# Kernel optimization log

Hardware: AMD Instinct MI355X
Metric: run time of the kernel (lower is better)

The kernel has to match this reference:

```python
import jax, jax.numpy as jnp
import numpy as np

D_MODEL = 1024
N_HEADS = 16
D_K = D_MODEL // N_HEADS


def setup_inputs() -> dict:
    key = jax.random.key(0)
    ks = jax.random.split(key, 9)
    s = 0.02
    x = jax.random.normal(ks[0], (2, 2048, D_MODEL), dtype=jnp.float32)
    Wq = jax.random.normal(ks[1], (D_MODEL, D_MODEL), dtype=jnp.float32) * s
    bq = jax.random.normal(ks[2], (D_MODEL,), dtype=jnp.float32) * s
    Wk = jax.random.normal(ks[3], (D_MODEL, D_MODEL), dtype=jnp.float32) * s
    bk = jax.random.normal(ks[4], (D_MODEL,), dtype=jnp.float32) * s
    Wv = jax.random.normal(ks[5], (D_MODEL, D_MODEL), dtype=jnp.float32) * s
    bv = jax.random.normal(ks[6], (D_MODEL,), dtype=jnp.float32) * s
    Wo = jax.random.normal(ks[7], (D_MODEL, D_MODEL), dtype=jnp.float32) * s
    bo = jax.random.normal(ks[8], (D_MODEL,), dtype=jnp.float32) * s
    return {"x": x, "Wq": Wq, "bq": bq, "Wk": Wk, "bk": bk,
            "Wv": Wv, "bv": bv, "Wo": Wo, "bo": bo}


def reference(x, Wq, bq, Wk, bk, Wv, bv, Wo, bo):
    B, S, D = x.shape
    # nn.Linear: y = x @ W.T + b
    q = x @ Wq.T + bq  # [B,S,D]
    k = x @ Wk.T + bk
    v = x @ Wv.T + bv
    # split heads -> [B,H,S,dk]
    q = q.reshape(B, S, N_HEADS, D_K).transpose(0, 2, 1, 3)
    k = k.reshape(B, S, N_HEADS, D_K).transpose(0, 2, 1, 3)
    v = v.reshape(B, S, N_HEADS, D_K).transpose(0, 2, 1, 3)
    scale = 1.0 / jnp.sqrt(jnp.asarray(D_K, dtype=x.dtype))
    scores = jnp.einsum('bhqd,bhkd->bhqk', q, k) * scale  # [B,H,S,S]
    weights = jax.nn.softmax(scores, axis=-1)
    out = jnp.einsum('bhqk,bhkd->bhqd', weights, v)  # [B,H,S,dk]
    concat = out.transpose(0, 2, 1, 3).reshape(B, S, D)
    return concat @ Wo.T + bo
```

## Files before the change

### kernel.cpp

```cpp
#include <hip/hip_runtime.h>

typedef unsigned short ushort_t;
typedef __attribute__((ext_vector_type(8))) __bf16 bf16x8;
typedef __attribute__((ext_vector_type(4))) float floatx4;

#define AS1 __attribute__((address_space(1)))
#define AS3 __attribute__((address_space(3)))

#define D_MODEL 1024
#define NH 16
#define DKH 64
#define SEQ 2048
#define NB 2
#define MTOT (NB * SEQ)

#define QSCALE 0.18033688011112042f

#define OFF_X   0u
#define OFF_WQ  4194304u
#define OFF_BQ  5242880u
#define OFF_WK  5243904u
#define OFF_BK  6292480u
#define OFF_WV  6293504u
#define OFF_BV  7342080u
#define OFF_WO  7343104u
#define OFF_BO  8391680u
#define CVT_TOT 8392704u

__device__ __forceinline__ float bf2f(ushort_t u) {
    union { unsigned u; float f; } v; v.u = ((unsigned)u) << 16; return v.f;
}
__device__ __forceinline__ ushort_t f2bf(float f) {
    union { float f; unsigned u; } v; v.f = f;
    unsigned r = v.u + 0x7FFFu + ((v.u >> 16) & 1u);
    return (ushort_t)(r >> 16);
}
__device__ __forceinline__ unsigned pack2bf(float a, float b) {
    unsigned ua = __float_as_uint(a), ub = __float_as_uint(b);
    ua = ua + 0x7FFFu + ((ua >> 16) & 1u);
    ub = ub + 0x7FFFu + ((ub >> 16) & 1u);
    return __builtin_amdgcn_perm(ub, ua, 0x07060302);
}
__device__ __forceinline__ float fexp2(float x) { return __builtin_amdgcn_exp2f(x); }

#define GSYNC(N) do { \
    asm volatile("s_waitcnt vmcnt(" #N ")" ::: "memory"); \
    __builtin_amdgcn_s_barrier(); \
    __builtin_amdgcn_sched_barrier(0); \
} while (0)

__global__ __launch_bounds__(256) void convert_kernel(
    const float* __restrict__ x,  const float* __restrict__ wq, const float* __restrict__ bq_,
    const float* __restrict__ wk, const float* __restrict__ bk_, const float* __restrict__ wv,
    const float* __restrict__ bv_, const float* __restrict__ wo, const float* __restrict__ bo_,
    ushort_t* __restrict__ dst)
{
    const unsigned idx = ((unsigned)blockIdx.x * 256u + threadIdx.x) * 4u;
    if (idx >= CVT_TOT) return;
    const float* src; unsigned off;
    if      (idx < OFF_WQ) { src = x;   off = idx - OFF_X;  }
    else if (idx < OFF_BQ) { src = wq;  off = idx - OFF_WQ; }
    else if (idx < OFF_WK) { src = bq_; off = idx - OFF_BQ; }
    else if (idx < OFF_BK) { src = wk;  off = idx - OFF_WK; }
    else if (idx < OFF_WV) { src = bk_; off = idx - OFF_BK; }
    else if (idx < OFF_BV) { src = wv;  off = idx - OFF_WV; }
    else if (idx < OFF_WO) { src = bv_; off = idx - OFF_BV; }
    else if (idx < OFF_BO) { src = wo;  off = idx - OFF_WO; }
    else                   { src = bo_; off = idx - OFF_BO; }
    float4 v = *reinterpret_cast<const float4*>(src + off);
    uint2 p;
    p.x = pack2bf(v.x, v.y);
    p.y = pack2bf(v.z, v.w);
    *reinterpret_cast<uint2*>(dst + idx) = p;
}

__device__ __forceinline__ void gemm_core(
    const ushort_t* __restrict__ X, const ushort_t* __restrict__ W,
    int m0, int n0, ushort_t* lds, floatx4 acc[4][4])
{
    const int tid = threadIdx.x;
    const int lane = tid & 63, wv = tid >> 6;
    const int wm = (wv >> 1) * 64, wn = (wv & 1) * 64;
    const int l15 = lane & 15, quad = lane >> 4;
    const floatx4 z4 = {0.f, 0.f, 0.f, 0.f};
#pragma unroll
    for (int i = 0; i < 4; ++i)
#pragma unroll
        for (int j = 0; j < 4; ++j) acc[i][j] = z4;
    const int lrow = lane >> 2;
    const int lcol = (lane & 3) * 8;
    const ushort_t* gA = X + (size_t)(m0 + lrow) * D_MODEL + lcol;
    const ushort_t* gB = W + (size_t)(n0 + lrow) * D_MODEL + lcol;

    auto STAGE = [&](ushort_t* Ln, int k0) {
#pragma unroll
        for (int j = 0; j < 2; ++j) {
            const int r0 = (wv * 2 + j) * 16;
            __builtin_amdgcn_global_load_lds(
                (const AS1 unsigned*)(gA + (size_t)r0 * D_MODEL + k0),
                (AS3 unsigned*)(Ln + r0 * 32), 16, 0, 0);
            __builtin_amdgcn_global_load_lds(
                (const AS1 unsigned*)(gB + (size_t)r0 * D_MODEL + k0),
                (AS3 unsigned*)(Ln + 4096 + r0 * 32), 16, 0, 0);
        }
    };
    auto COMPUTE = [&](const ushort_t* L) {
        bf16x8 af[4], bfr[4];
#pragma unroll
        for (int i = 0; i < 4; ++i)
            af[i] = *reinterpret_cast<const bf16x8*>(L + (wm + i * 16 + l15) * 32 + quad * 8);
#pragma unroll
        for (int j = 0; j < 4; ++j)
            bfr[j] = *reinterpret_cast<const bf16x8*>(L + 4096 + (wn + j * 16 + l15) * 32 + quad * 8);
#pragma unroll
        for (int i = 0; i < 4; ++i)
#pragma unroll
            for (int j = 0; j < 4; ++j)
                acc[i][j] = __builtin_amdgcn_mfma_f32_16x16x32_bf16(af[i], bfr[j], acc[i][j], 0, 0, 0);
    };

    ushort_t* b0 = lds;
    ushort_t* b1 = lds + 8192;
    ushort_t* b2 = lds + 16384;

    STAGE(b0, 0);
    STAGE(b1, 32);
    for (int tt = 0; tt < 30; tt += 3) {
        GSYNC(4); STAGE(b2, (tt + 2) * 32); COMPUTE(b0);
        GSYNC(4); STAGE(b0, (tt + 3) * 32); COMPUTE(b1);
        GSYNC(4); STAGE(b1, (tt + 4) * 32); COMPUTE(b2);
    }
    GSYNC(4); COMPUTE(b0);
    GSYNC(0); COMPUTE(b1);
}

__global__ __launch_bounds__(256, 3) void qkv_kernel(
    const ushort_t* __restrict__ x,
    const ushort_t* __restrict__ Wq, const ushort_t* __restrict__ bq,
    const ushort_t* __restrict__ Wk, const ushort_t* __restrict__ bk,
    const ushort_t* __restrict__ Wv, const ushort_t* __restrict__ bv,
    ushort_t* __restrict__ q_ws, ushort_t* __restrict__ k_ws, ushort_t* __restrict__ vt_ws)
{
    __shared__ __align__(16) ushort_t lds[24576];
    const int L = blockIdx.x;
    const int m_idx = (L & 7) + 8 * ((L >> 3) & 3);
    const int y = L >> 5;
    const int m0 = m_idx * 128;
    const int which = y >> 3;
    const int n0 = (y & 7) * 128;
    const ushort_t* W    = (which == 0) ? Wq : (which == 1) ? Wk : Wv;
    const ushort_t* bias = (which == 0) ? bq : (which == 1) ? bk : bv;
    floatx4 acc[4][4];
    gemm_core(x, W, m0, n0, lds, acc);
    const int tid = threadIdx.x, lane = tid & 63, wv = tid >> 6;
    const int wm = (wv >> 1) * 64, wn = (wv & 1) * 64;
    const int l15 = lane & 15, quad = lane >> 4;
    const int b0 = m0 >> 11;
    const int s0 = m0 & (SEQ - 1);
    __syncthreads();
    if (which < 2) {
        ushort_t* Ts = lds;
        ushort_t* dst = (which == 0) ? q_ws : k_ws;
        const float scl = (which == 0) ? QSCALE : 1.0f;
#pragma unroll
        for (int j = 0; j < 4; ++j) {
            int coln = wn + j * 16 + l15;
            float bb = bf2f(bias[n0 + coln]);
#pragma unroll
            for (int i = 0; i < 4; ++i)
#pragma unroll
                for (int r = 0; r < 4; ++r) {
                    int rowm = wm + i * 16 + quad * 4 + r;
                    Ts[rowm * 136 + coln] = f2bf((acc[i][j][r] + bb) * scl);
                }
        }
        __syncthreads();
#pragma unroll
        for (int i = 0; i < 8; ++i) {
            int c = tid + 256 * i;
            int rowm = c >> 4, chunk = c & 15;
            float4 v = *reinterpret_cast<const float4*>(Ts + rowm * 136 + chunk * 8);
            int s = s0 + rowm;
            int n = n0 + chunk * 8, h = n >> 6, d = n & 63;
            *reinterpret_cast<float4*>(dst + (((size_t)(b0 * NH + h)) * SEQ + s) * DKH + d) = v;
        }
    } else {
        ushort_t* Ts = lds;
#pragma unroll
        for (int j = 0; j < 4; ++j) {
            int coln = wn + j * 16 + l15;
            float bb = bf2f(bias[n0 + coln]);
#pragma unroll
            for (int i = 0; i < 4; ++i)
#pragma unroll
                for (int r = 0; r < 4; ++r) {
                    int rowm = wm + i * 16 + quad * 4 + r;
                    Ts[coln * 136 + rowm] = f2bf(acc[i][j][r] + bb);
                }
        }
        __syncthreads();
#pragma unroll
        for (int i = 0; i < 8; ++i) {
            int c = tid + 256 * i;
            int nr = c >> 4, mc = (c & 15) * 8;
            float4 v = *reinterpret_cast<const float4*>(Ts + nr * 136 + mc);
            int n = n0 + nr, h = n >> 6, d = n & 63;
            *reinterpret_cast<float4*>(vt_ws + (((size_t)(b0 * NH + h)) * DKH + d) * SEQ + s0 + mc) = v;
        }
    }
}

__global__ __launch_bounds__(512, 4) void attn_kernel(
    const ushort_t* __restrict__ q_ws, const ushort_t* __restrict__ k_ws,
    const ushort_t* __restrict__ vt_ws, ushort_t* __restrict__ concat)
{
    __shared__ __align__(16) ushort_t sm[36864];
    const int L = blockIdx.x;
    const int qb = (L >> 3) & 15;
    const int bh = (L & 7) + ((L >> 7) << 3);
    const int tid = threadIdx.x;
    const int lane = tid & 63, wv = tid >> 6;
    const int half = wv >> 2, wq = wv & 3;
    const int l15 = lane & 15, quad = lane >> 4;
    const int ht = tid & 255;

    const ushort_t* Qg = q_ws + ((size_t)bh * SEQ + qb * 128) * DKH;
    const ushort_t* Kg = k_ws + ((size_t)bh * SEQ + half * (SEQ / 2)) * DKH;
    const ushort_t* Vg = vt_ws + (size_t)bh * DKH * SEQ + half * (SEQ / 2);

    ushort_t* Ks     = sm + half * 4608;
    ushort_t* VTs    = sm + 9216 + half * 4608;
    ushort_t* Ps     = sm + 18432 + wv * 2304;
    ushort_t* Qstage = sm + 18432;

    const int r0c = ht >> 3,         c0c = (ht & 7) * 8;
    const int r1c = (ht + 256) >> 3, c1c = ((ht + 256) & 7) * 8;

#pragma unroll
    for (int i = 0; i < 2; ++i) {
        int c = tid + 512 * i;
        int row = c >> 3, col = (c & 7) * 8;
        *reinterpret_cast<float4*>(Qstage + row * 72 + col) =
            *reinterpret_cast<const float4*>(Qg + row * DKH + col);
    }
    __syncthreads();
    bf16x8 aq[2][2];
#pragma unroll
    for (int nt = 0; nt < 2; ++nt)
#pragma unroll
        for (int ks = 0; ks < 2; ++ks)
            aq[nt][ks] = *reinterpret_cast<const bf16x8*>(Qstage + (wq * 32 + nt * 16 + l15) * 72 + ks * 32 + quad * 8);

    const floatx4 z4 = {0.f, 0.f, 0.f, 0.f};
    floatx4 o[2][4];
    floatx4 la4[2] = {z4, z4};
#pragma unroll
    for (int nt = 0; nt < 2; ++nt)
#pragma unroll
        for (int dt = 0; dt < 4; ++dt) o[nt][dt] = z4;

    float4 pk0 = *reinterpret_cast<const float4*>(Kg + (size_t)r0c * DKH + c0c);
    float4 pk1 = *reinterpret_cast<const float4*>(Kg + (size_t)r1c * DKH + c1c);
    float4 pv0 = *reinterpret_cast<const float4*>(Vg + (size_t)r0c * SEQ + c0c);
    float4 pv1 = *reinterpret_cast<const float4*>(Vg + (size_t)r1c * SEQ + c1c);

    for (int t = 0; t < 16; ++t) {
        __syncthreads();
        *reinterpret_cast<float4*>(Ks + r0c * 72 + c0c) = pk0;
        *reinterpret_cast<float4*>(Ks + r1c * 72 + c1c) = pk1;
        *reinterpret_cast<float4*>(VTs + r0c * 72 + c0c) = pv0;
        *reinterpret_cast<float4*>(VTs + r1c * 72 + c1c) = pv1;
        __syncthreads();
        if (t < 15) {
            int toff = (t + 1) * 64;
            pk0 = *reinterpret_cast<const float4*>(Kg + (size_t)(toff + r0c) * DKH + c0c);
            pk1 = *reinterpret_cast<const float4*>(Kg + (size_t)(toff + r1c) * DKH + c1c);
            pv0 = *reinterpret_cast<const float4*>(Vg + (size_t)r0c * SEQ + toff + c0c);
            pv1 = *reinterpret_cast<const float4*>(Vg + (size_t)r1c * SEQ + toff + c1c);
        }

        floatx4 st[2][4];
#pragma unroll
        for (int mt = 0; mt < 4; ++mt) {
            bf16x8 akf = *reinterpret_cast<const bf16x8*>(Ks + (mt * 16 + l15) * 72 + quad * 8);
            st[0][mt] = __builtin_amdgcn_mfma_f32_16x16x32_bf16(akf, aq[0][0], z4, 0, 0, 0);
            st[1][mt] = __builtin_amdgcn_mfma_f32_16x16x32_bf16(akf, aq[1][0], z4, 0, 0, 0);
        }
#pragma unroll
        for (int mt = 0; mt < 4; ++mt) {
            bf16x8 akf = *reinterpret_cast<const bf16x8*>(Ks + (mt * 16 + l15) * 72 + 32 + quad * 8);
            st[0][mt] = __builtin_amdgcn_mfma_f32_16x16x32_bf16(akf, aq[0][1], st[0][mt], 0, 0, 0);
            st[1][mt] = __builtin_amdgcn_mfma_f32_16x16x32_bf16(akf, aq[1][1], st[1][mt], 0, 0, 0);
        }

#pragma unroll
        for (int nt = 0; nt < 2; ++nt)
#pragma unroll
            for (int mt = 0; mt < 4; ++mt) {
#pragma unroll
                for (int r = 0; r < 4; ++r) st[nt][mt][r] = fexp2(st[nt][mt][r]);
                la4[nt] += st[nt][mt];
                uint2 pk;
                pk.x = pack2bf(st[nt][mt][0], st[nt][mt][1]);
                pk.y = pack2bf(st[nt][mt][2], st[nt][mt][3]);
                *reinterpret_cast<uint2*>(Ps + (nt * 16 + l15) * 72 + mt * 16 + quad * 4) = pk;
            }
        asm volatile("s_waitcnt lgkmcnt(0)" ::: "memory");
#pragma unroll
        for (int ks = 0; ks < 2; ++ks) {
            bf16x8 ap0 = *reinterpret_cast<const bf16x8*>(Ps + l15 * 72 + ks * 32 + quad * 8);
            bf16x8 ap1 = *reinterpret_cast<const bf16x8*>(Ps + (16 + l15) * 72 + ks * 32 + quad * 8);
#pragma unroll
            for (int dt = 0; dt < 4; ++dt) {
                bf16x8 bvv = *reinterpret_cast<const bf16x8*>(VTs + (dt * 16 + l15) * 72 + ks * 32 + quad * 8);
                o[0][dt] = __builtin_amdgcn_mfma_f32_16x16x32_bf16(ap0, bvv, o[0][dt], 0, 0, 0);
                o[1][dt] = __builtin_amdgcn_mfma_f32_16x16x32_bf16(ap1, bvv, o[1][dt], 0, 0, 0);
            }
        }
    }
    float lsum[2];
#pragma unroll
    for (int nt = 0; nt < 2; ++nt) {
        float s = la4[nt][0] + la4[nt][1] + la4[nt][2] + la4[nt][3];
        s += __shfl_xor(s, 16, 64);
        s += __shfl_xor(s, 32, 64);
        lsum[nt] = s;
    }
    __syncthreads();
    float* Of = (float*)sm;
    float* lf = Of + 128 * 68;
    if (half == 1) {
#pragma unroll
        for (int nt = 0; nt < 2; ++nt) {
            if (quad == 0) lf[wq * 32 + nt * 16 + l15] = lsum[nt];
#pragma unroll
            for (int r = 0; r < 4; ++r) {
                int row = wq * 32 + nt * 16 + quad * 4 + r;
#pragma unroll
                for (int dt = 0; dt < 4; ++dt)
                    Of[row * 68 + dt * 16 + l15] = o[nt][dt][r];
            }
        }
    }
    __syncthreads();
    if (half == 0) {
        const int b0 = bh >> 4, h = bh & 15;
#pragma unroll
        for (int nt = 0; nt < 2; ++nt) {
            float ltot = lsum[nt] + lf[wq * 32 + nt * 16 + l15];
            float linv = 1.f / ltot;
#pragma unroll
            for (int r = 0; r < 4; ++r) {
                float lB = __shfl(linv, quad * 4 + r, 64);
                int row = wq * 32 + nt * 16 + quad * 4 + r;
                size_t base = ((size_t)(b0 * SEQ + qb * 128 + row)) * D_MODEL + h * DKH;
#pragma unroll
                for (int dt = 0; dt < 4; ++dt) {
                    float sum = o[nt][dt][r] + Of[row * 68 + dt * 16 + l15];
                    concat[base + dt * 16 + l15] = f2bf(sum * lB);
                }
            }
        }
    }
}

__global__ __launch_bounds__(256, 3) void oproj_kernel(
    const ushort_t* __restrict__ cc, const ushort_t* __restrict__ Wo,
    const ushort_t* __restrict__ bo, float* __restrict__ out)
{
    __shared__ __align__(16) ushort_t lds[24576];
    const int L = blockIdx.x;
    const int m_idx = (L & 7) + 8 * (L >> 6);
    const int n_idx = (L >> 3) & 7;
    const int m0 = m_idx * 128, n0 = n_idx * 128;
    floatx4 acc[4][4];
    gemm_core(cc, Wo, m0, n0, lds, acc);
    const int tid = threadIdx.x, lane = tid & 63, wv = tid >> 6;
    const int wm = (wv >> 1) * 64, wn = (wv & 1) * 64;
    const int l15 = lane & 15, quad = lane >> 4;
#pragma unroll
    for (int j = 0; j < 4; ++j) {
        int n = n0 + wn + j * 16 + l15;
        float bb = bf2f(bo[n]);
#pragma unroll
        for (int i = 0; i < 4; ++i)
#pragma unroll
            for (int r = 0; r < 4; ++r) {
                int m = m0 + wm + i * 16 + quad * 4 + r;
                out[(size_t)m * D_MODEL + n] = acc[i][j][r] + bb;
            }
    }
}

extern "C" void kernel_launch(void* const* d_in, const int* in_sizes, int n_in,
                              void* d_out, int out_size, void* d_ws, size_t ws_size,
                              hipStream_t stream)
{
    ushort_t* cvt = (ushort_t*)d_ws;
    const ushort_t* xb  = cvt + OFF_X;
    const ushort_t* Wqb = cvt + OFF_WQ;
    const ushort_t* bqb = cvt + OFF_BQ;
    const ushort_t* Wkb = cvt + OFF_WK;
    const ushort_t* bkb = cvt + OFF_BK;
    const ushort_t* Wvb = cvt + OFF_WV;
    const ushort_t* bvb = cvt + OFF_BV;
    const ushort_t* Wob = cvt + OFF_WO;
    const ushort_t* bob = cvt + OFF_BO;
    ushort_t* q_ws   = cvt + CVT_TOT;
    ushort_t* k_ws   = q_ws  + (size_t)MTOT * D_MODEL;
    ushort_t* vt_ws  = k_ws  + (size_t)MTOT * D_MODEL;
    ushort_t* concat = vt_ws + (size_t)MTOT * D_MODEL;

    convert_kernel<<<(CVT_TOT / 1024), 256, 0, stream>>>(
        (const float*)d_in[0], (const float*)d_in[1], (const float*)d_in[2],
        (const float*)d_in[3], (const float*)d_in[4], (const float*)d_in[5],
        (const float*)d_in[6], (const float*)d_in[7], (const float*)d_in[8], cvt);
    qkv_kernel<<<dim3(768), 256, 0, stream>>>(xb, Wqb, bqb, Wkb, bkb, Wvb, bvb, q_ws, k_ws, vt_ws);
    attn_kernel<<<dim3(512), 512, 0, stream>>>(q_ws, k_ws, vt_ws, concat);
    oproj_kernel<<<dim3(256), 256, 0, stream>>>(concat, Wob, bob, (float*)d_out);
}
```

Baseline: 190.2 us.

## Enlarge QKV GEMM tiles to 256x128 and use eight-wave blocks for output projection

The QKV projection now runs 512-thread blocks that each compute a 256x128 tile, with triple-buffered LDS stages sized for the taller A tile. A new block-to-tile mapping assigns consecutive N tiles to the same XCD so x rows are shared within an XCD's cache. The output projection keeps 128x128 tiles but spreads them over eight waves, each computing 64x32, which gives more latency hiding per block. The larger QKV tiles reuse each B tile across more rows, but they halve the block count to 384, which may load the CUs unevenly, and they raise LDS use per block.

New measurement: 193.2 us. No clear change (+1.6%).

```diff
diff --git a/kernel.cpp b/kernel.cpp
--- a/kernel.cpp
+++ b/kernel.cpp
@@ -74,7 +74,7 @@
     *reinterpret_cast<uint2*>(dst + idx) = p;
 }
 
-__device__ __forceinline__ void gemm_core(
+__device__ __forceinline__ void gemm_core_qkv(
     const ushort_t* __restrict__ X, const ushort_t* __restrict__ W,
     int m0, int n0, ushort_t* lds, floatx4 acc[4][4])
 {
@@ -95,14 +95,15 @@
     auto STAGE = [&](ushort_t* Ln, int k0) {
 #pragma unroll
         for (int j = 0; j < 2; ++j) {
-            const int r0 = (wv * 2 + j) * 16;
+            const int rA = (wv * 2 + j) * 16;
             __builtin_amdgcn_global_load_lds(
-                (const AS1 unsigned*)(gA + (size_t)r0 * D_MODEL + k0),
-                (AS3 unsigned*)(Ln + r0 * 32), 16, 0, 0);
-            __builtin_amdgcn_global_load_lds(
-                (const AS1 unsigned*)(gB + (size_t)r0 * D_MODEL + k0),
-                (AS3 unsigned*)(Ln + 4096 + r0 * 32), 16, 0, 0);
-        }
+                (const AS1 unsigned*)(gA + (size_t)rA * D_MODEL + k0),
+                (AS3 unsigned*)(Ln + rA * 32), 16, 0, 0);
+        }
+        const int rB = wv * 16;
+        __builtin_amdgcn_global_load_lds(
+            (const AS1 unsigned*)(gB + (size_t)rB * D_MODEL + k0),
+            (AS3 unsigned*)(Ln + 8192 + rB * 32), 16, 0, 0);
     };
     auto COMPUTE = [&](const ushort_t* L) {
         bf16x8 af[4], bfr[4];
@@ -111,7 +112,7 @@
             af[i] = *reinterpret_cast<const bf16x8*>(L + (wm + i * 16 + l15) * 32 + quad * 8);
 #pragma unroll
         for (int j = 0; j < 4; ++j)
-            bfr[j] = *reinterpret_cast<const bf16x8*>(L + 4096 + (wn + j * 16 + l15) * 32 + quad * 8);
+            bfr[j] = *reinterpret_cast<const bf16x8*>(L + 8192 + (wn + j * 16 + l15) * 32 + quad * 8);
 #pragma unroll
         for (int i = 0; i < 4; ++i)
 #pragma unroll
@@ -120,38 +121,39 @@
     };
 
     ushort_t* b0 = lds;
-    ushort_t* b1 = lds + 8192;
-    ushort_t* b2 = lds + 16384;
-
+    ushort_t* b1 = lds + 12288;
+    ushort_t* b2 = lds + 24576;
     STAGE(b0, 0);
     STAGE(b1, 32);
     for (int tt = 0; tt < 30; tt += 3) {
-        GSYNC(4); STAGE(b2, (tt + 2) * 32); COMPUTE(b0);
-        GSYNC(4); STAGE(b0, (tt + 3) * 32); COMPUTE(b1);
-        GSYNC(4); STAGE(b1, (tt + 4) * 32); COMPUTE(b2);
-    }
-    GSYNC(4); COMPUTE(b0);
+        GSYNC(3); STAGE(b2, (tt + 2) * 32); COMPUTE(b0);
+        GSYNC(3); STAGE(b0, (tt + 3) * 32); COMPUTE(b1);
+        GSYNC(3); STAGE(b1, (tt + 4) * 32); COMPUTE(b2);
+    }
+    GSYNC(3); COMPUTE(b0);
     GSYNC(0); COMPUTE(b1);
 }
 
-__global__ __launch_bounds__(256, 3) void qkv_kernel(
+__global__ __launch_bounds__(512, 2) void qkv_kernel(
     const ushort_t* __restrict__ x,
     const ushort_t* __restrict__ Wq, const ushort_t* __restrict__ bq,
     const ushort_t* __restrict__ Wk, const ushort_t* __restrict__ bk,
     const ushort_t* __restrict__ Wv, const ushort_t* __restrict__ bv,
     ushort_t* __restrict__ q_ws, ushort_t* __restrict__ k_ws, ushort_t* __restrict__ vt_ws)
 {
-    __shared__ __align__(16) ushort_t lds[24576];
+    __shared__ __align__(16) ushort_t lds[36864];
     const int L = blockIdx.x;
-    const int m_idx = (L & 7) + 8 * ((L >> 3) & 3);
-    const int y = L >> 5;
-    const int m0 = m_idx * 128;
-    const int which = y >> 3;
-    const int n0 = (y & 7) * 128;
+    const int xcd = L & 7;
+    const int r = L >> 3;
+    const int n_idx = xcd * 3 + (r % 3);
+    const int m_idx = r / 3;
+    const int m0 = m_idx * 256;
+    const int which = n_idx >> 3;
+    const int n0 = (n_idx & 7) * 128;
     const ushort_t* W    = (which == 0) ? Wq : (which == 1) ? Wk : Wv;
     const ushort_t* bias = (which == 0) ? bq : (which == 1) ? bk : bv;
     floatx4 acc[4][4];
-    gemm_core(x, W, m0, n0, lds, acc);
+    gemm_core_qkv(x, W, m0, n0, lds, acc);
     const int tid = threadIdx.x, lane = tid & 63, wv = tid >> 6;
     const int wm = (wv >> 1) * 64, wn = (wv & 1) * 64;
     const int l15 = lane & 15, quad = lane >> 4;
@@ -169,15 +171,15 @@
 #pragma unroll
             for (int i = 0; i < 4; ++i)
 #pragma unroll
-                for (int r = 0; r < 4; ++r) {
-                    int rowm = wm + i * 16 + quad * 4 + r;
-                    Ts[rowm * 136 + coln] = f2bf((acc[i][j][r] + bb) * scl);
+                for (int rr = 0; rr < 4; ++rr) {
+                    int rowm = wm + i * 16 + quad * 4 + rr;
+                    Ts[rowm * 136 + coln] = f2bf((acc[i][j][rr] + bb) * scl);
                 }
         }
         __syncthreads();
 #pragma unroll
         for (int i = 0; i < 8; ++i) {
-            int c = tid + 256 * i;
+            int c = tid + 512 * i;
             int rowm = c >> 4, chunk = c & 15;
             float4 v = *reinterpret_cast<const float4*>(Ts + rowm * 136 + chunk * 8);
             int s = s0 + rowm;
@@ -193,17 +195,17 @@
 #pragma unroll
             for (int i = 0; i < 4; ++i)
 #pragma unroll
-                for (int r = 0; r < 4; ++r) {
-                    int rowm = wm + i * 16 + quad * 4 + r;
-                    Ts[coln * 136 + rowm] = f2bf(acc[i][j][r] + bb);
+                for (int rr = 0; rr < 4; ++rr) {
+                    int rowm = wm + i * 16 + quad * 4 + rr;
+                    Ts[coln * 264 + rowm] = f2bf(acc[i][j][rr] + bb);
                 }
         }
         __syncthreads();
 #pragma unroll
         for (int i = 0; i < 8; ++i) {
-            int c = tid + 256 * i;
-            int nr = c >> 4, mc = (c & 15) * 8;
-            float4 v = *reinterpret_cast<const float4*>(Ts + nr * 136 + mc);
+            int c = tid + 512 * i;
+            int nr = c >> 5, mc = (c & 31) * 8;
+            float4 v = *reinterpret_cast<const float4*>(Ts + nr * 264 + mc);
             int n = n0 + nr, h = n >> 6, d = n & 63;
             *reinterpret_cast<float4*>(vt_ws + (((size_t)(b0 * NH + h)) * DKH + d) * SEQ + s0 + mc) = v;
         }
@@ -298,7 +300,7 @@
 #pragma unroll
             for (int mt = 0; mt < 4; ++mt) {
 #pragma unroll
-                for (int r = 0; r < 4; ++r) st[nt][mt][r] = fexp2(st[nt][mt][r]);
+                for (int rr = 0; rr < 4; ++rr) st[nt][mt][rr] = fexp2(st[nt][mt][rr]);
                 la4[nt] += st[nt][mt];
                 uint2 pk;
                 pk.x = pack2bf(st[nt][mt][0], st[nt][mt][1]);
@@ -334,11 +336,11 @@
         for (int nt = 0; nt < 2; ++nt) {
             if (quad == 0) lf[wq * 32 + nt * 16 + l15] = lsum[nt];
 #pragma unroll
-            for (int r = 0; r < 4; ++r) {
-                int row = wq * 32 + nt * 16 + quad * 4 + r;
+            for (int rr = 0; rr < 4; ++rr) {
+                int row = wq * 32 + nt * 16 + quad * 4 + rr;
 #pragma unroll
                 for (int dt = 0; dt < 4; ++dt)
-                    Of[row * 68 + dt * 16 + l15] = o[nt][dt][r];
+                    Of[row * 68 + dt * 16 + l15] = o[nt][dt][rr];
             }
         }
     }
@@ -350,13 +352,13 @@
             float ltot = lsum[nt] + lf[wq * 32 + nt * 16 + l15];
             float linv = 1.f / ltot;
 #pragma unroll
-            for (int r = 0; r < 4; ++r) {
-                float lB = __shfl(linv, quad * 4 + r, 64);
-                int row = wq * 32 + nt * 16 + quad * 4 + r;
+            for (int rr = 0; rr < 4; ++rr) {
+                float lB = __shfl(linv, quad * 4 + rr, 64);
+                int row = wq * 32 + nt * 16 + quad * 4 + rr;
                 size_t base = ((size_t)(b0 * SEQ + qb * 128 + row)) * D_MODEL + h * DKH;
 #pragma unroll
                 for (int dt = 0; dt < 4; ++dt) {
-                    float sum = o[nt][dt][r] + Of[row * 68 + dt * 16 + l15];
+                    float sum = o[nt][dt][rr] + Of[row * 68 + dt * 16 + l15];
                     concat[base + dt * 16 + l15] = f2bf(sum * lB);
                 }
             }
@@ -364,30 +366,76 @@
     }
 }
 
-__global__ __launch_bounds__(256, 3) void oproj_kernel(
+__global__ __launch_bounds__(512, 2) void oproj_kernel(
     const ushort_t* __restrict__ cc, const ushort_t* __restrict__ Wo,
     const ushort_t* __restrict__ bo, float* __restrict__ out)
 {
     __shared__ __align__(16) ushort_t lds[24576];
     const int L = blockIdx.x;
-    const int m_idx = (L & 7) + 8 * (L >> 6);
-    const int n_idx = (L >> 3) & 7;
-    const int m0 = m_idx * 128, n0 = n_idx * 128;
-    floatx4 acc[4][4];
-    gemm_core(cc, Wo, m0, n0, lds, acc);
-    const int tid = threadIdx.x, lane = tid & 63, wv = tid >> 6;
-    const int wm = (wv >> 1) * 64, wn = (wv & 1) * 64;
+    const int n0 = (L & 7) * 128;
+    const int m0 = (L >> 3) * 128;
+    const int tid = threadIdx.x;
+    const int lane = tid & 63, wv = tid >> 6;
+    const int wm = (wv >> 2) * 64, wn = (wv & 3) * 32;
     const int l15 = lane & 15, quad = lane >> 4;
-#pragma unroll
-    for (int j = 0; j < 4; ++j) {
+    const floatx4 z4 = {0.f, 0.f, 0.f, 0.f};
+    floatx4 acc[4][2];
+#pragma unroll
+    for (int i = 0; i < 4; ++i)
+#pragma unroll
+        for (int j = 0; j < 2; ++j) acc[i][j] = z4;
+    const int lrow = lane >> 2;
+    const int lcol = (lane & 3) * 8;
+    const ushort_t* gA = cc + (size_t)(m0 + lrow) * D_MODEL + lcol;
+    const ushort_t* gB = Wo + (size_t)(n0 + lrow) * D_MODEL + lcol;
+
+    auto STAGE = [&](ushort_t* Ln, int k0) {
+        const int r0 = wv * 16;
+        __builtin_amdgcn_global_load_lds(
+            (const AS1 unsigned*)(gA + (size_t)r0 * D_MODEL + k0),
+            (AS3 unsigned*)(Ln + r0 * 32), 16, 0, 0);
+        __builtin_amdgcn_global_load_lds(
+            (const AS1 unsigned*)(gB + (size_t)r0 * D_MODEL + k0),
+            (AS3 unsigned*)(Ln + 4096 + r0 * 32), 16, 0, 0);
+    };
+    auto COMPUTE = [&](const ushort_t* Lb) {
+        bf16x8 af[4], bfr[2];
+#pragma unroll
+        for (int i = 0; i < 4; ++i)
+            af[i] = *reinterpret_cast<const bf16x8*>(Lb + (wm + i * 16 + l15) * 32 + quad * 8);
+#pragma unroll
+        for (int j = 0; j < 2; ++j)
+            bfr[j] = *reinterpret_cast<const bf16x8*>(Lb + 4096 + (wn + j * 16 + l15) * 32 + quad * 8);
+#pragma unroll
+        for (int i = 0; i < 4; ++i)
+#pragma unroll
+            for (int j = 0; j < 2; ++j)
+                acc[i][j] = __builtin_amdgcn_mfma_f32_16x16x32_bf16(af[i], bfr[j], acc[i][j], 0, 0, 0);
+    };
+
+    ushort_t* b0 = lds;
+    ushort_t* b1 = lds + 8192;
+    ushort_t* b2 = lds + 16384;
+    STAGE(b0, 0);
+    STAGE(b1, 32);
+    for (int tt = 0; tt < 30; tt += 3) {
+        GSYNC(2); STAGE(b2, (tt + 2) * 32); COMPUTE(b0);
+        GSYNC(2); STAGE(b0, (tt + 3) * 32); COMPUTE(b1);
+        GSYNC(2); STAGE(b1, (tt + 4) * 32); COMPUTE(b2);
+    }
+    GSYNC(2); COMPUTE(b0);
+    GSYNC(0); COMPUTE(b1);
+
+#pragma unroll
+    for (int j = 0; j < 2; ++j) {
         int n = n0 + wn + j * 16 + l15;
         float bb = bf2f(bo[n]);
 #pragma unroll
         for (int i = 0; i < 4; ++i)
 #pragma unroll
-            for (int r = 0; r < 4; ++r) {
-                int m = m0 + wm + i * 16 + quad * 4 + r;
-                out[(size_t)m * D_MODEL + n] = acc[i][j][r] + bb;
+            for (int rr = 0; rr < 4; ++rr) {
+                int m = m0 + wm + i * 16 + quad * 4 + rr;
+                out[(size_t)m * D_MODEL + n] = acc[i][j][rr] + bb;
             }
     }
 }
@@ -415,7 +463,7 @@
         (const float*)d_in[0], (const float*)d_in[1], (const float*)d_in[2],
         (const float*)d_in[3], (const float*)d_in[4], (const float*)d_in[5],
         (const float*)d_in[6], (const float*)d_in[7], (const float*)d_in[8], cvt);
-    qkv_kernel<<<dim3(768), 256, 0, stream>>>(xb, Wqb, bqb, Wkb, bkb, Wvb, bvb, q_ws, k_ws, vt_ws);
+    qkv_kernel<<<dim3(384), 512, 0, stream>>>(xb, Wqb, bqb, Wkb, bkb, Wvb, bvb, q_ws, k_ws, vt_ws);
     attn_kernel<<<dim3(512), 512, 0, stream>>>(q_ws, k_ws, vt_ws, concat);
-    oproj_kernel<<<dim3(256), 256, 0, stream>>>(concat, Wob, bob, (float*)d_out);
-}
+    oproj_kernel<<<dim3(256), 512, 0, stream>>>(concat, Wob, bob, (float*)d_out);
+}
```
